# Performance work log

Measured on AMD Instinct MI355X. Metric: run time of the kernel, lower is better.

The kernel has to match this reference:

```python
import jax, jax.numpy as jnp
import numpy as np
import math

# (mul, l, parity) per irrep block
IRREPS1 = [(64, 0, 1), (64, 1, -1), (64, 2, 1)]
IRREPS2 = [(1, 0, 1), (1, 1, -1), (1, 2, 1), (1, 3, -1)]
BATCH = 20000


def _f(n):
    return math.factorial(round(n))


def _su2_cg(j1, j2, j3):
    """Clebsch-Gordan coefficients <j1 m1 j2 m2 | j3 m3> (complex SH basis, Racah formula)."""
    C = np.zeros((2 * j1 + 1, 2 * j2 + 1, 2 * j3 + 1))
    for m1 in range(-j1, j1 + 1):
        for m2 in range(-j2, j2 + 1):
            m3 = m1 + m2
            if abs(m3) > j3:
                continue
            pref = math.sqrt((2 * j3 + 1) * _f(j3 + j1 - j2) * _f(j3 - j1 + j2) * _f(j1 + j2 - j3) / _f(j1 + j2 + j3 + 1))
            pref *= math.sqrt(_f(j3 + m3) * _f(j3 - m3) * _f(j1 - m1) * _f(j1 + m1) * _f(j2 - m2) * _f(j2 + m2))
            s = 0.0
            for k in range(0, j1 + j2 - j3 + 1):
                d = [k, j1 + j2 - j3 - k, j1 - m1 - k, j2 + m2 - k, j3 - j2 + m1 + k, j3 - j1 - m2 + k]
                if min(d) < 0:
                    continue
                s += (-1) ** k / np.prod([float(_f(t)) for t in d])
            C[j1 + m1, j2 + m2, j3 + m3] = pref * s
    return C


def _q_real_to_complex(l):
    q = np.zeros((2 * l + 1, 2 * l + 1), dtype=np.complex128)
    for m in range(-l, 0):
        q[l + m, l + abs(m)] = 1 / math.sqrt(2)
        q[l + m, l - abs(m)] = -1j / math.sqrt(2)
    q[l, l] = 1
    for m in range(1, l + 1):
        q[l + m, l + abs(m)] = (-1) ** m / math.sqrt(2)
        q[l + m, l - abs(m)] = 1j * (-1) ** m / math.sqrt(2)
    return (-1j) ** l * q  # phase makes the real-basis CG real


def _w3j(l1, l2, l3):
    """Real-spherical-harmonic Wigner 3j tensor, Frobenius-normalized to 1 (e3nn convention)."""
    Q1, Q2, Q3 = _q_real_to_complex(l1), _q_real_to_complex(l2), _q_real_to_complex(l3)
    C = _su2_cg(l1, l2, l3).astype(np.complex128)
    C = np.einsum('ij,kl,mn,ikm->jln', Q1, Q2, np.conj(Q3).T, C)
    C = np.real(C)
    return C / np.linalg.norm(C)


def _slices(irreps):
    s, out = 0, []
    for mul, l, p in irreps:
        d = mul * (2 * l + 1)
        out.append((s, s + d))
        s += d
    return out


def _build_paths():
    paths = []  # (i1, i2, l3, p3)
    for i1, (mul1, l1, p1) in enumerate(IRREPS1):
        for i2, (mul2, l2, p2) in enumerate(IRREPS2):
            for l3 in range(abs(l1 - l2), l1 + l2 + 1):
                paths.append((i1, i2, l3, p1 * p2))
    # stable sort of output irreps: by l, with the "natural" parity (-1)^l first (e3nn order)
    order = sorted(range(len(paths)), key=lambda i: (paths[i][2], -paths[i][3] * (-1) ** paths[i][2]))
    return paths, order


def setup_inputs() -> dict:
    key = jax.random.key(0)
    k1, k2 = jax.random.split(key)
    d1 = sum(mul * (2 * l + 1) for mul, l, _ in IRREPS1)
    d2 = sum(mul * (2 * l + 1) for mul, l, _ in IRREPS2)
    x = jax.random.normal(k1, (BATCH, d1), dtype=jnp.float32)
    y = jax.random.normal(k2, (BATCH, d2), dtype=jnp.float32)
    return {"x": x, "y": y}


def reference(x, y):
    sl1, sl2 = _slices(IRREPS1), _slices(IRREPS2)
    paths, order = _build_paths()
    chunks = [None] * len(paths)
    for idx, (i1, i2, l3, p3) in enumerate(paths):
        mul1, l1, _ = IRREPS1[i1]
        mul2, l2, _ = IRREPS2[i2]
        a, b = sl1[i1]
        c, d = sl2[i2]
        x1 = x[:, a:b].reshape(-1, mul1, 2 * l1 + 1)   # [B, u, 2l1+1]
        x2 = y[:, c:d].reshape(-1, mul2, 2 * l2 + 1)   # [B, v, 2l2+1]
        w = jnp.asarray(_w3j(l1, l2, l3), dtype=x.dtype)  # [2l1+1, 2l2+1, 2l3+1]
        alpha = math.sqrt(2 * l3 + 1)  # 'component' irrep normalization
        z = alpha * jnp.einsum('ijk,bui,bvj->buvk', w, x1, x2)  # uvuv mode
        chunks[idx] = z.reshape(z.shape[0], -1)
    return jnp.concatenate([chunks[i] for i in order], axis=1)
```

## Files before the change

kernel.cpp:

```cpp
#include <hip/hip_runtime.h>


#define CEXPR __host__ __device__ constexpr

struct Cplx { double re, im; };
CEXPR Cplx cmul(Cplx a, Cplx b){ return {a.re*b.re - a.im*b.im, a.re*b.im + a.im*b.re}; }
CEXPR Cplx cadd(Cplx a, Cplx b){ return {a.re+b.re, a.im+b.im}; }
CEXPR Cplx cconj(Cplx a){ return {a.re, -a.im}; }
CEXPR Cplx cscale(double s, Cplx a){ return {s*a.re, s*a.im}; }

CEXPR double cfact(int n){ double r = 1.0; for (int i = 2; i <= n; ++i) r *= (double)i; return r; }

CEXPR double csqrt_(double x){
  if (x <= 0.0) return 0.0;
  double g = x > 1.0 ? x : 1.0;
  for (int i = 0; i < 80; ++i) g = 0.5*(g + x/g);
  return g;
}

struct CGT { double c[5][7][11]; };

CEXPR CGT su2_cg(int j1, int j2, int j3){
  CGT T{};
  for (int m1 = -j1; m1 <= j1; ++m1){
    for (int m2 = -j2; m2 <= j2; ++m2){
      int m3 = m1 + m2;
      if (m3 < -j3 || m3 > j3) continue;
      double pref = csqrt_((double)(2*j3+1) * cfact(j3+j1-j2) * cfact(j3-j1+j2)
                           * cfact(j1+j2-j3) / cfact(j1+j2+j3+1));
      pref *= csqrt_(cfact(j3+m3)*cfact(j3-m3)*cfact(j1-m1)*cfact(j1+m1)*cfact(j2-m2)*cfact(j2+m2));
      double s = 0.0;
      for (int k = 0; k <= j1+j2-j3; ++k){
        int d1 = j1+j2-j3-k, d2 = j1-m1-k, d3 = j2+m2-k, d4 = j3-j2+m1+k, d5 = j3-j1-m2+k;
        if (d1 < 0 || d2 < 0 || d3 < 0 || d4 < 0 || d5 < 0) continue;
        double denom = cfact(k)*cfact(d1)*cfact(d2)*cfact(d3)*cfact(d4)*cfact(d5);
        s += ((k & 1) ? -1.0 : 1.0) / denom;
      }
      T.c[j1+m1][j2+m2][j3+m3] = pref * s;
    }
  }
  return T;
}

struct QM { Cplx q[11][11]; };

CEXPR QM qmat(int l){
  QM Q{};
  const double is2 = csqrt_(0.5);
  for (int m = -l; m < 0; ++m){
    Q.q[l+m][l-m] = Cplx{is2, 0.0};
    Q.q[l+m][l+m] = Cplx{0.0, -is2};
  }
  Q.q[l][l] = Cplx{1.0, 0.0};
  for (int m = 1; m <= l; ++m){
    double sg = (m & 1) ? -1.0 : 1.0;
    Q.q[l+m][l+m] = Cplx{sg*is2, 0.0};
    Q.q[l+m][l-m] = Cplx{0.0, sg*is2};
  }
  Cplx ph{1.0, 0.0};
  for (int i = 0; i < (l & 3); ++i) ph = cmul(ph, Cplx{0.0, -1.0});
  for (int r = 0; r < 2*l+1; ++r)
    for (int c = 0; c < 2*l+1; ++c)
      Q.q[r][c] = cmul(ph, Q.q[r][c]);
  return Q;
}

struct W3T { double w[5][7][11]; };

CEXPR W3T w3j_tensor(int l1, int l2, int l3){
  CGT cg = su2_cg(l1, l2, l3);
  QM Q1 = qmat(l1);
  QM Q2 = qmat(l2);
  QM Q3 = qmat(l3);
  const int n1 = 2*l1+1, n2 = 2*l2+1, n3 = 2*l3+1;
  W3T R{};
  double nrm2 = 0.0;
  for (int j = 0; j < n1; ++j){
    for (int l = 0; l < n2; ++l){
      for (int n = 0; n < n3; ++n){
        Cplx s{0.0, 0.0};
        for (int i = 0; i < n1; ++i){
          Cplx q1 = Q1.q[i][j];
          if (q1.re == 0.0 && q1.im == 0.0) continue;
          for (int k = 0; k < n2; ++k){
            Cplx q2 = Q2.q[k][l];
            if (q2.re == 0.0 && q2.im == 0.0) continue;
            int m = (i - l1) + (k - l2) + l3;
            if (m < 0 || m >= n3) continue;
            double cgv = cg.c[i][k][m];
            if (cgv == 0.0) continue;
            Cplx q3 = cconj(Q3.q[n][m]);
            if (q3.re == 0.0 && q3.im == 0.0) continue;
            s = cadd(s, cscale(cgv, cmul(cmul(q1, q2), q3)));
          }
        }
        R.w[j][l][n] = s.re;
        nrm2 += s.re * s.re;
      }
    }
  }
  double scale = csqrt_((double)(2*l3+1)) / csqrt_(nrm2);
  for (int j = 0; j < n1; ++j)
    for (int l = 0; l < n2; ++l)
      for (int n = 0; n < n3; ++n){
        double v = R.w[j][l][n] * scale;
        R.w[j][l][n] = (v > 1e-10 || v < -1e-10) ? v : 0.0;
      }
  return R;
}


typedef float fv2 __attribute__((ext_vector_type(2), aligned(4)));
typedef float fv4 __attribute__((ext_vector_type(4), aligned(4)));

template<int L1, int L2, int L3>
__device__ __forceinline__ void do_path(const float* xv, const float* yv, float* __restrict__ op){
  static constexpr W3T W = w3j_tensor(L1, L2, L3);
  constexpr int N1 = 2*L1+1, N2 = 2*L2+1, N3 = 2*L3+1;
  float r[N3];
  #pragma unroll
  for (int k = 0; k < N3; ++k){
    float acc = 0.0f;
    #pragma unroll
    for (int i = 0; i < N1; ++i){
      #pragma unroll
      for (int j = 0; j < N2; ++j){
        const float c = (float)W.w[i][j][k];
        if (c != 0.0f) acc = fmaf(c, xv[i]*yv[j], acc);
      }
    }
    r[k] = acc;
  }
  constexpr int K4 = N3 & ~3;
  #pragma unroll
  for (int k = 0; k < K4; k += 4){
    fv4 v; v.x = r[k]; v.y = r[k+1]; v.z = r[k+2]; v.w = r[k+3];
    *(fv4*)(op + k) = v;
  }
  if constexpr ((N3 & 3) >= 2){
    fv2 v; v.x = r[K4]; v.y = r[K4+1];
    *(fv2*)(op + K4) = v;
  }
  if constexpr ((N3 & 1) == 1){
    op[N3-1] = r[N3-1];
  }
}

__global__ __launch_bounds__(256) void tp_kernel(const float* __restrict__ x,
                                                 const float* __restrict__ y,
                                                 float* __restrict__ out,
                                                 int rows)
{
  const int u   = threadIdx.x & 63;
  const int row = blockIdx.x * 4 + (threadIdx.x >> 6);
  if (row >= rows) return;

  const float* xr = x + (size_t)row * 576;
  const float* yr = y + (size_t)row * 16;

  float x0[1], x1[3], x2[5];
  x0[0] = xr[u];
  { fv2 t = *(const fv2*)(xr + 64 + 3*u);  x1[0] = t.x; x1[1] = t.y; x1[2] = xr[64 + 3*u + 2]; }
  { fv4 t = *(const fv4*)(xr + 256 + 5*u); x2[0] = t.x; x2[1] = t.y; x2[2] = t.z; x2[3] = t.w;
    x2[4] = xr[256 + 5*u + 4]; }

  float yv[16];
  #pragma unroll
  for (int q = 0; q < 4; ++q){
    fv4 t = *(const fv4*)(yr + 4*q);
    yv[4*q] = t.x; yv[4*q+1] = t.y; yv[4*q+2] = t.z; yv[4*q+3] = t.w;
  }
  const float* y0 = yv;
  const float* y1 = yv + 1;
  const float* y2 = yv + 4;
  const float* y3 = yv + 9;

  float* o = out + (size_t)row * 9216;

  do_path<0,0,0>(x0, y0, o + 0    + u*1);
  do_path<0,1,1>(x0, y1, o + 192  + u*3);
  do_path<0,2,2>(x0, y2, o + 1536 + u*5);
  do_path<0,3,3>(x0, y3, o + 4096 + u*7);

  do_path<1,0,1>(x1, y0, o + 384  + u*3);
  do_path<1,1,0>(x1, y1, o + 64   + u*1);
  do_path<1,1,1>(x1, y1, o + 1152 + u*3);
  do_path<1,1,2>(x1, y1, o + 1856 + u*5);
  do_path<1,2,1>(x1, y2, o + 576  + u*3);
  do_path<1,2,2>(x1, y2, o + 3136 + u*5);
  do_path<1,2,3>(x1, y2, o + 4544 + u*7);
  do_path<1,3,2>(x1, y3, o + 2176 + u*5);
  do_path<1,3,3>(x1, y3, o + 5888 + u*7);
  do_path<1,3,4>(x1, y3, o + 6784 + u*9);

  do_path<2,0,2>(x2, y0, o + 2496 + u*5);
  do_path<2,1,1>(x2, y1, o + 768  + u*3);
  do_path<2,1,2>(x2, y1, o + 3456 + u*5);
  do_path<2,1,3>(x2, y1, o + 4992 + u*7);
  do_path<2,2,0>(x2, y2, o + 128  + u*1);
  do_path<2,2,1>(x2, y2, o + 1344 + u*3);
  do_path<2,2,2>(x2, y2, o + 2816 + u*5);
  do_path<2,2,3>(x2, y2, o + 6336 + u*7);
  do_path<2,2,4>(x2, y2, o + 7360 + u*9);
  do_path<2,3,1>(x2, y3, o + 960  + u*3);
  do_path<2,3,2>(x2, y3, o + 3776 + u*5);
  do_path<2,3,3>(x2, y3, o + 5440 + u*7);
  do_path<2,3,4>(x2, y3, o + 7936 + u*9);
  do_path<2,3,5>(x2, y3, o + 8512 + u*11);
}

extern "C" void kernel_launch(void* const* d_in, const int* in_sizes, int n_in,
                              void* d_out, int out_size, void* d_ws, size_t ws_size,
                              hipStream_t stream)
{
  const float* x = (const float*)d_in[0];
  const float* y = (const float*)d_in[1];
  float* out = (float*)d_out;
  const int rows = in_sizes[0] / 576;
  const int blocks = (rows + 3) / 4;
  hipLaunchKernelGGL(tp_kernel, dim3(blocks), dim3(256), 0, stream, x, y, out, rows);
}
```

Measured before the change: 802.3 us.

## Stage path outputs in LDS and flush with coalesced 16-byte stores

Each wavefront now writes per-path results into its own LDS buffer and then copies them to global memory as contiguous float4 stores spread across lanes, in four batches. Before, each lane wrote strided 3-to-11-float chunks. Scalar output paths are still stored directly. The aim is fully coalesced writes for this store-bound kernel, at the cost of LDS round trips, waitcnt fences and about 40KB of shared memory per block, which may limit occupancy.

```diff
diff --git a/kernel.cpp b/kernel.cpp
--- a/kernel.cpp
+++ b/kernel.cpp
@@ -110,14 +110,20 @@
 }
 
 
-typedef float fv2 __attribute__((ext_vector_type(2), aligned(4)));
-typedef float fv4 __attribute__((ext_vector_type(4), aligned(4)));
+typedef float fv2  __attribute__((ext_vector_type(2), aligned(4)));
+typedef float fv4  __attribute__((ext_vector_type(4), aligned(4)));
+typedef float fv4a __attribute__((ext_vector_type(4), aligned(16)));
+
+__device__ __forceinline__ void lds_fence(){
+  asm volatile("s_waitcnt lgkmcnt(0)" ::: "memory");
+  __builtin_amdgcn_sched_barrier(0);
+}
 
 template<int L1, int L2, int L3>
-__device__ __forceinline__ void do_path(const float* xv, const float* yv, float* __restrict__ op){
+__device__ __forceinline__ void path_stage(const float* xv, const float* yv,
+                                           float* __restrict__ seg, int u){
   static constexpr W3T W = w3j_tensor(L1, L2, L3);
   constexpr int N1 = 2*L1+1, N2 = 2*L2+1, N3 = 2*L3+1;
-  float r[N3];
   #pragma unroll
   for (int k = 0; k < N3; ++k){
     float acc = 0.0f;
@@ -129,31 +135,56 @@
         if (c != 0.0f) acc = fmaf(c, xv[i]*yv[j], acc);
       }
     }
-    r[k] = acc;
-  }
-  constexpr int K4 = N3 & ~3;
-  #pragma unroll
-  for (int k = 0; k < K4; k += 4){
-    fv4 v; v.x = r[k]; v.y = r[k+1]; v.z = r[k+2]; v.w = r[k+3];
-    *(fv4*)(op + k) = v;
-  }
-  if constexpr ((N3 & 3) >= 2){
-    fv2 v; v.x = r[K4]; v.y = r[K4+1];
-    *(fv2*)(op + K4) = v;
-  }
-  if constexpr ((N3 & 1) == 1){
-    op[N3-1] = r[N3-1];
-  }
-}
+    seg[u*N3 + k] = acc;
+  }
+}
+
+template<int N3>
+__device__ __forceinline__ void path_flush(const float* __restrict__ seg,
+                                           float* __restrict__ gout, int u){
+  constexpr int NCH = (N3 + 3) / 4;
+  #pragma unroll
+  for (int c = 0; c < NCH; ++c){
+    const int idx = c*256 + 4*u;
+    if ((c + 1) * 4 <= N3  || u < 16 * (N3 - 4*c)){
+      fv4a v = *(const fv4a*)(seg + idx);
+      *(fv4a*)(gout + idx) = v;
+    }
+  }
+}
+
+template<int L1, int L2>
+__device__ __forceinline__ void path_direct0(const float* xv, const float* yv,
+                                             float* __restrict__ op, int u){
+  static constexpr W3T W = w3j_tensor(L1, L2, 0);
+  constexpr int N1 = 2*L1+1, N2 = 2*L2+1;
+  float acc = 0.0f;
+  #pragma unroll
+  for (int i = 0; i < N1; ++i){
+    #pragma unroll
+    for (int j = 0; j < N2; ++j){
+      const float c = (float)W.w[i][j][0];
+      if (c != 0.0f) acc = fmaf(c, xv[i]*yv[j], acc);
+    }
+  }
+  op[u] = acc;
+}
+
+#define BATCH_CAP 39
 
 __global__ __launch_bounds__(256) void tp_kernel(const float* __restrict__ x,
                                                  const float* __restrict__ y,
                                                  float* __restrict__ out,
                                                  int rows)
 {
+  __shared__ __align__(16) float lds[4][BATCH_CAP * 64];
+
   const int u   = threadIdx.x & 63;
-  const int row = blockIdx.x * 4 + (threadIdx.x >> 6);
+  const int w   = threadIdx.x >> 6;
+  const int row = blockIdx.x * 4 + w;
   if (row >= rows) return;
+
+  float* wb = lds[w];
 
   const float* xr = x + (size_t)row * 576;
   const float* yr = y + (size_t)row * 16;
@@ -177,36 +208,70 @@
 
   float* o = out + (size_t)row * 9216;
 
-  do_path<0,0,0>(x0, y0, o + 0    + u*1);
-  do_path<0,1,1>(x0, y1, o + 192  + u*3);
-  do_path<0,2,2>(x0, y2, o + 1536 + u*5);
-  do_path<0,3,3>(x0, y3, o + 4096 + u*7);
-
-  do_path<1,0,1>(x1, y0, o + 384  + u*3);
-  do_path<1,1,0>(x1, y1, o + 64   + u*1);
-  do_path<1,1,1>(x1, y1, o + 1152 + u*3);
-  do_path<1,1,2>(x1, y1, o + 1856 + u*5);
-  do_path<1,2,1>(x1, y2, o + 576  + u*3);
-  do_path<1,2,2>(x1, y2, o + 3136 + u*5);
-  do_path<1,2,3>(x1, y2, o + 4544 + u*7);
-  do_path<1,3,2>(x1, y3, o + 2176 + u*5);
-  do_path<1,3,3>(x1, y3, o + 5888 + u*7);
-  do_path<1,3,4>(x1, y3, o + 6784 + u*9);
-
-  do_path<2,0,2>(x2, y0, o + 2496 + u*5);
-  do_path<2,1,1>(x2, y1, o + 768  + u*3);
-  do_path<2,1,2>(x2, y1, o + 3456 + u*5);
-  do_path<2,1,3>(x2, y1, o + 4992 + u*7);
-  do_path<2,2,0>(x2, y2, o + 128  + u*1);
-  do_path<2,2,1>(x2, y2, o + 1344 + u*3);
-  do_path<2,2,2>(x2, y2, o + 2816 + u*5);
-  do_path<2,2,3>(x2, y2, o + 6336 + u*7);
-  do_path<2,2,4>(x2, y2, o + 7360 + u*9);
-  do_path<2,3,1>(x2, y3, o + 960  + u*3);
-  do_path<2,3,2>(x2, y3, o + 3776 + u*5);
-  do_path<2,3,3>(x2, y3, o + 5440 + u*7);
-  do_path<2,3,4>(x2, y3, o + 7936 + u*9);
-  do_path<2,3,5>(x2, y3, o + 8512 + u*11);
+  path_direct0<0,0>(x0, y0, o + 0,   u);
+  path_direct0<1,1>(x1, y1, o + 64,  u);
+  path_direct0<2,2>(x2, y2, o + 128, u);
+
+  path_stage<0,1,1>(x0, y1, wb +  0*64, u);
+  path_stage<0,2,2>(x0, y2, wb +  3*64, u);
+  path_stage<0,3,3>(x0, y3, wb +  8*64, u);
+  path_stage<1,0,1>(x1, y0, wb + 15*64, u);
+  path_stage<1,1,1>(x1, y1, wb + 18*64, u);
+  path_stage<1,1,2>(x1, y1, wb + 21*64, u);
+  path_stage<1,2,1>(x1, y2, wb + 26*64, u);
+  path_stage<1,2,2>(x1, y2, wb + 29*64, u);
+  lds_fence();
+  path_flush<3>(wb +  0*64, o + 192,  u);
+  path_flush<5>(wb +  3*64, o + 1536, u);
+  path_flush<7>(wb +  8*64, o + 4096, u);
+  path_flush<3>(wb + 15*64, o + 384,  u);
+  path_flush<3>(wb + 18*64, o + 1152, u);
+  path_flush<5>(wb + 21*64, o + 1856, u);
+  path_flush<3>(wb + 26*64, o + 576,  u);
+  path_flush<5>(wb + 29*64, o + 3136, u);
+  lds_fence();
+
+  path_stage<1,2,3>(x1, y2, wb +  0*64, u);
+  path_stage<1,3,2>(x1, y3, wb +  7*64, u);
+  path_stage<1,3,3>(x1, y3, wb + 12*64, u);
+  path_stage<1,3,4>(x1, y3, wb + 19*64, u);
+  path_stage<2,0,2>(x2, y0, wb + 28*64, u);
+  path_stage<2,1,1>(x2, y1, wb + 33*64, u);
+  lds_fence();
+  path_flush<7>(wb +  0*64, o + 4544, u);
+  path_flush<5>(wb +  7*64, o + 2176, u);
+  path_flush<7>(wb + 12*64, o + 5888, u);
+  path_flush<9>(wb + 19*64, o + 6784, u);
+  path_flush<5>(wb + 28*64, o + 2496, u);
+  path_flush<3>(wb + 33*64, o + 768,  u);
+  lds_fence();
+
+  path_stage<2,1,2>(x2, y1, wb +  0*64, u);
+  path_stage<2,1,3>(x2, y1, wb +  5*64, u);
+  path_stage<2,2,1>(x2, y2, wb + 12*64, u);
+  path_stage<2,2,2>(x2, y2, wb + 15*64, u);
+  path_stage<2,2,3>(x2, y2, wb + 20*64, u);
+  path_stage<2,2,4>(x2, y2, wb + 27*64, u);
+  path_stage<2,3,1>(x2, y3, wb + 36*64, u);
+  lds_fence();
+  path_flush<5>(wb +  0*64, o + 3456, u);
+  path_flush<7>(wb +  5*64, o + 4992, u);
+  path_flush<3>(wb + 12*64, o + 1344, u);
+  path_flush<5>(wb + 15*64, o + 2816, u);
+  path_flush<7>(wb + 20*64, o + 6336, u);
+  path_flush<9>(wb + 27*64, o + 7360, u);
+  path_flush<3>(wb + 36*64, o + 960,  u);
+  lds_fence();
+
+  path_stage<2,3,2>(x2, y3, wb +  0*64, u);
+  path_stage<2,3,3>(x2, y3, wb +  5*64, u);
+  path_stage<2,3,4>(x2, y3, wb + 12*64, u);
+  path_stage<2,3,5>(x2, y3, wb + 21*64, u);
+  lds_fence();
+  path_flush<5> (wb +  0*64, o + 3776, u);
+  path_flush<7> (wb +  5*64, o + 5440, u);
+  path_flush<9> (wb + 12*64, o + 7936, u);
+  path_flush<11>(wb + 21*64, o + 8512, u);
 }
 
 extern "C" void kernel_launch(void* const* d_in, const int* in_sizes, int n_in,
```

After: 754.2 us. 6.0% less time.
